# Kernel optimization log

Measured on AMD Instinct MI355X. Metric: run time of the kernel, lower is better.

The kernel has to match this reference:

```python
import jax, jax.numpy as jnp
import numpy as np

NUM_HEADS = 8

def setup_inputs() -> dict:
    key = jax.random.key(0)
    ks = jax.random.split(key, 6)
    B, nW, F_W, ED = 8, 64, 128, 512
    x = jax.random.normal(ks[0], (B * nW, F_W, ED), dtype=jnp.float32)
    adj_mask = jax.random.normal(ks[1], (B, NUM_HEADS, F_W, F_W), dtype=jnp.float32)
    qkv_w = jax.random.normal(ks[2], (ED, 3 * ED), dtype=jnp.float32) * (ED ** -0.5)
    qkv_b = jax.random.normal(ks[3], (3 * ED,), dtype=jnp.float32) * 0.02
    proj_w = jax.random.normal(ks[4], (ED, ED), dtype=jnp.float32) * (ED ** -0.5)
    proj_b = jax.random.normal(ks[5], (ED,), dtype=jnp.float32) * 0.02
    return {"x": x, "adj_mask": adj_mask, "qkv_w": qkv_w, "qkv_b": qkv_b,
            "proj_w": proj_w, "proj_b": proj_b, "B": B, "nW": nW}

def reference(x, adj_mask, qkv_w, qkv_b, proj_w, proj_b, B, nW):
    B_nW, F_W, ED = x.shape
    H = NUM_HEADS
    hd = ED // H
    scale = hd ** -0.5
    # qkv projection: [B_nW, F_W, 3, H, hd]
    qkv = (x @ qkv_w + qkv_b).reshape(B_nW, F_W, 3, H, hd)
    qkv = jnp.transpose(qkv, (2, 0, 3, 1, 4))  # [3, B_nW, H, F_W, hd]
    q, k, v = qkv[0], qkv[1], qkv[2]
    attn = jnp.einsum('bhqd,bhkd->bhqk', q * scale, k)  # [B_nW, H, F_W, F_W]
    # additive adjacency mask, broadcast over windows
    attn = attn.reshape(B, nW, H, F_W, F_W) + adj_mask[:, None]
    attn = attn.reshape(B_nW, H, F_W, F_W)
    attn = jax.nn.softmax(attn, axis=-1)
    out = jnp.einsum('bhqk,bhkd->bhqd', attn, v)  # [B_nW, H, F_W, hd]
    out = jnp.transpose(out, (0, 2, 1, 3)).reshape(B_nW, F_W, ED)
    return out @ proj_w + proj_b
```

## Files before the change

### kernel.cpp

```cpp
#include <hip/hip_runtime.h>

typedef __bf16 bf16_t;
typedef __bf16 bf16x8 __attribute__((ext_vector_type(8)));
typedef float f32x4 __attribute__((ext_vector_type(4)));
typedef float f32x16 __attribute__((ext_vector_type(16)));

#define MFMA16(a, b, c) __builtin_amdgcn_mfma_f32_16x16x32_bf16(a, b, c, 0, 0, 0)
#define MFMA32(a, b, c) __builtin_amdgcn_mfma_f32_32x32x16_bf16(a, b, c, 0, 0, 0)

#define F_W 128
#define ED 512
#define NH 8
#define HD 64
#define B_NW 512
#define NTOK 65536

typedef const __attribute__((address_space(1))) void gvoid_t;
typedef __attribute__((address_space(3))) void lvoid_t;
__device__ __forceinline__ void gload16(const void* g, void* l) {
    __builtin_amdgcn_global_load_lds((gvoid_t*)g, (lvoid_t*)l, 16, 0, 0);
}

__global__ __launch_bounds__(256) void prep_kernel(
    const float* __restrict__ qkv_w,
    const float* __restrict__ proj_w,
    bf16_t* __restrict__ qkv_wt,
    bf16_t* __restrict__ proj_wt) {
    int idx = blockIdx.x * 256 + threadIdx.x;
    if (idx < 1536 * 512) {
        int n = idx >> 9, k = idx & 511;
        qkv_wt[idx] = (bf16_t)qkv_w[k * 1536 + n];
    }
    if (idx < 512 * 512) {
        int n = idx >> 9, k = idx & 511;
        proj_wt[idx] = (bf16_t)proj_w[k * 512 + n];
    }
}

__global__ __launch_bounds__(256) void prep_x_kernel(
    const float* __restrict__ x, bf16_t* __restrict__ xbf) {
    size_t i = ((size_t)blockIdx.x * 256 + threadIdx.x) * 8;
    float4 v0 = *(const float4*)(x + i);
    float4 v1 = *(const float4*)(x + i + 4);
    bf16x8 o = {(bf16_t)v0.x, (bf16_t)v0.y, (bf16_t)v0.z, (bf16_t)v0.w,
                (bf16_t)v1.x, (bf16_t)v1.y, (bf16_t)v1.z, (bf16_t)v1.w};
    *(bf16x8*)(xbf + i) = o;
}

__global__ __launch_bounds__(256, 4) void qkv_gemm_kernel(
    const bf16_t* __restrict__ xbf,
    const bf16_t* __restrict__ qkv_wt,
    const float* __restrict__ qkv_b,
    bf16_t* qk_ws,
    bf16_t* vt_ws) {
    __shared__ __align__(16) char sm[32768];
    bf16_t* x_s = (bf16_t*)sm;
    bf16_t* w_s = (bf16_t*)(sm + 16384);
    bf16_t* tb  = (bf16_t*)sm;

    const int tid = threadIdx.x;
    const int wave = tid >> 6, lane = tid & 63;
    const int l31 = lane & 31, lhi = lane >> 5;
    const int wm = wave >> 1, wn = wave & 1;
    const int bid = blockIdx.x;
    const int idx = bid >> 3;
    const int mt_l = idx / 12;
    const int nt = idx - mt_l * 12;
    const int mtile = (bid & 7) * 64 + mt_l;
    const size_t m0 = (size_t)mtile * 128;
    const int n0 = nt * 128;

    const int srow = lane >> 3;
    const int scol = ((lane & 7) * 8) ^ ((srow & 7) << 3);

    f32x16 acc[2][2];
#pragma unroll
    for (int mf = 0; mf < 2; ++mf)
#pragma unroll
        for (int nf = 0; nf < 2; ++nf) acc[mf][nf] = (f32x16)0.0f;

    for (int kc = 0; kc < 8; ++kc) {
        const int k0 = kc * 64;
        __syncthreads();
#pragma unroll
        for (int i = 0; i < 4; ++i) {
            int c = wave * 4 + i;
            gload16(xbf + (m0 + c * 8 + srow) * 512 + k0 + scol, x_s + c * 512);
        }
#pragma unroll
        for (int i = 0; i < 4; ++i) {
            int c = wave * 4 + i;
            gload16(qkv_wt + (size_t)(n0 + c * 8 + srow) * 512 + k0 + scol,
                    w_s + c * 512);
        }
        __syncthreads();

#pragma unroll
        for (int ks = 0; ks < 4; ++ks) {
            bf16x8 a[2], b[2];
#pragma unroll
            for (int mf = 0; mf < 2; ++mf) {
                int row = wm * 64 + mf * 32 + l31;
                a[mf] = *(const bf16x8*)(x_s + row * 64 +
                                         ((ks * 16 + lhi * 8) ^ ((row & 7) << 3)));
            }
#pragma unroll
            for (int nf = 0; nf < 2; ++nf) {
                int rw = wn * 64 + nf * 32 + l31;
                b[nf] = *(const bf16x8*)(w_s + rw * 64 +
                                         ((ks * 16 + lhi * 8) ^ ((rw & 7) << 3)));
            }
#pragma unroll
            for (int mf = 0; mf < 2; ++mf)
#pragma unroll
                for (int nf = 0; nf < 2; ++nf)
                    acc[mf][nf] = MFMA32(a[mf], b[nf], acc[mf][nf]);
        }
    }

    if (nt < 8) {
        const float scale = (nt < 4) ? 0.125f : 1.0f;
#pragma unroll
        for (int nf = 0; nf < 2; ++nf) {
            int col = n0 + wn * 64 + nf * 32 + l31;
            float bv = qkv_b[col];
#pragma unroll
            for (int mf = 0; mf < 2; ++mf)
#pragma unroll
                for (int j = 0; j < 16; ++j) {
                    int r = wm * 64 + mf * 32 + (j & 3) + 8 * (j >> 2) + 4 * lhi;
                    qk_ws[(m0 + r) * 1024 + col] =
                        (bf16_t)((acc[mf][nf][j] + bv) * scale);
                }
        }
    } else {
#pragma unroll
        for (int hh = 0; hh < 2; ++hh) {
            int h = (nt - 8) * 2 + hh;
            __syncthreads();
            if (wn == hh) {
#pragma unroll
                for (int nf = 0; nf < 2; ++nf) {
                    int d = nf * 32 + l31;
                    float bv = qkv_b[n0 + hh * 64 + d];
#pragma unroll
                    for (int mf = 0; mf < 2; ++mf)
#pragma unroll
                        for (int j = 0; j < 16; ++j) {
                            int r = wm * 64 + mf * 32 + (j & 3) + 8 * (j >> 2) + 4 * lhi;
                            tb[r * 72 + d] = (bf16_t)(acc[mf][nf][j] + bv);
                        }
                }
            }
            __syncthreads();
            {
                int d = tid & 63;
                int kh = tid >> 6;
                bf16_t* outp = vt_ws + ((size_t)(mtile * 8 + h) * 64 + d) * 128 + kh * 32;
#pragma unroll
                for (int o = 0; o < 4; ++o) {
                    bf16x8 v;
#pragma unroll
                    for (int e = 0; e < 8; ++e)
                        v[e] = tb[(kh * 32 + o * 8 + e) * 72 + d];
                    *(bf16x8*)(outp + o * 8) = v;
                }
            }
        }
    }
}

__global__ __launch_bounds__(512, 4) void attn_kernel(
    bf16_t* qk_ws,
    const bf16_t* __restrict__ vt_ws,
    const float* __restrict__ adj) {
    __shared__ __align__(16) char sm[32768];
    bf16_t* k_lds  = (bf16_t*)sm;
    bf16_t* vt_lds = (bf16_t*)(sm + 16384);
    bf16_t* pbuf   = (bf16_t*)sm;

    const int tid = threadIdx.x;
    const int wave = tid >> 6, lane = tid & 63;
    const int lrow = lane & 15, lgrp = lane >> 4;
    const int bid = blockIdx.x;
    const int w = (bid & 7) * 64 + (bid >> 6);
    const int h = (bid >> 3) & 7;
    const int bidx = bid & 7;

    bf16_t* qrow = qk_ws + (size_t)w * 128 * 1024;

    {
        const int krow_l = lane >> 3;
        const int kcol_l = ((lane & 7) * 8) ^ ((krow_l & 7) << 3);
#pragma unroll
        for (int i = 0; i < 2; ++i) {
            int c = wave * 2 + i;
            gload16(qrow + (size_t)(c * 8 + krow_l) * 1024 + 512 + h * 64 + kcol_l,
                    k_lds + c * 512);
        }
    }
    {
        const bf16_t* vtb = vt_ws + (size_t)(w * 8 + h) * 64 * 128;
        const int vrow_l = lane >> 4;
#pragma unroll
        for (int i = 0; i < 2; ++i) {
            int c = wave * 2 + i;
            int d = c * 4 + vrow_l;
            int vcol = ((lane & 15) * 8) ^ ((d & 7) << 3);
            gload16(vtb + (size_t)d * 128 + vcol, vt_lds + c * 512);
        }
    }
    bf16x8 aq[2];
    {
        int row = wave * 16 + lrow;
#pragma unroll
        for (int kb = 0; kb < 2; ++kb)
            aq[kb] = *(const bf16x8*)(qrow + (size_t)row * 1024 + h * 64 + kb * 32 + lgrp * 8);
    }
    __syncthreads();

    f32x4 sacc[8];
#pragma unroll
    for (int nf = 0; nf < 8; ++nf) sacc[nf] = (f32x4)0.0f;
#pragma unroll
    for (int kb = 0; kb < 2; ++kb) {
        bf16x8 b[8];
#pragma unroll
        for (int nf = 0; nf < 8; ++nf) {
            int row = nf * 16 + lrow;
            b[nf] = *(const bf16x8*)(k_lds + row * 64 + ((kb * 32 + lgrp * 8) ^ ((row & 7) << 3)));
        }
#pragma unroll
        for (int nf = 0; nf < 8; ++nf)
            sacc[nf] = MFMA16(aq[kb], b[nf], sacc[nf]);
    }

    const float* mbase = adj + ((size_t)(bidx * NH + h)) * F_W * F_W;
#pragma unroll
    for (int j = 0; j < 4; ++j) {
        int row = wave * 16 + lgrp * 4 + j;
        const float* mrow = mbase + (size_t)row * F_W;
        float mx = -1e30f;
#pragma unroll
        for (int nf = 0; nf < 8; ++nf) {
            sacc[nf][j] += mrow[nf * 16 + lrow];
            mx = fmaxf(mx, sacc[nf][j]);
        }
#pragma unroll
        for (int d = 1; d < 16; d <<= 1) mx = fmaxf(mx, __shfl_xor(mx, d));
        float sum = 0.f;
#pragma unroll
        for (int nf = 0; nf < 8; ++nf) {
            float p = exp2f((sacc[nf][j] - mx) * 1.44269504f);
            sacc[nf][j] = p;
            sum += p;
        }
#pragma unroll
        for (int d = 1; d < 16; d <<= 1) sum += __shfl_xor(sum, d);
        float r = 1.0f / sum;
#pragma unroll
        for (int nf = 0; nf < 8; ++nf) sacc[nf][j] *= r;
    }
    __syncthreads();

    f32x4 oacc[4];
#pragma unroll
    for (int nf = 0; nf < 4; ++nf) oacc[nf] = (f32x4)0.0f;

#pragma unroll
    for (int kb = 0; kb < 4; ++kb) {
#pragma unroll
        for (int nn = 0; nn < 2; ++nn) {
            int nf = kb * 2 + nn;
            int kk = nn * 16 + lrow;
#pragma unroll
            for (int j = 0; j < 4; ++j) {
                int r = wave * 16 + lgrp * 4 + j;
                pbuf[r * 40 + kk] = (bf16_t)(sacc[nf][j]);
            }
        }
        __syncthreads();
        bf16x8 a = *(const bf16x8*)(pbuf + (wave * 16 + lrow) * 40 + lgrp * 8);
        bf16x8 b[4];
#pragma unroll
        for (int nf = 0; nf < 4; ++nf) {
            int d = nf * 16 + lrow;
            b[nf] = *(const bf16x8*)(vt_lds + d * 128 + ((kb * 32 + lgrp * 8) ^ ((d & 7) << 3)));
        }
#pragma unroll
        for (int nf = 0; nf < 4; ++nf)
            oacc[nf] = MFMA16(a, b[nf], oacc[nf]);
        __syncthreads();
    }

#pragma unroll
    for (int nf = 0; nf < 4; ++nf) {
        int ocol = h * 64 + nf * 16 + lrow;
#pragma unroll
        for (int j = 0; j < 4; ++j) {
            int r = wave * 16 + lgrp * 4 + j;
            qrow[(size_t)r * 1024 + ocol] = (bf16_t)oacc[nf][j];
        }
    }
}

__global__ __launch_bounds__(256, 4) void proj_kernel(
    const bf16_t* __restrict__ a_g,
    const bf16_t* __restrict__ bt_g,
    const float* __restrict__ bias,
    float* __restrict__ out) {
    __shared__ __align__(16) char sm_[32768];
    bf16_t* a_s = (bf16_t*)sm_;
    bf16_t* b_s = (bf16_t*)(sm_ + 16384);
    const int tid = threadIdx.x;
    const int wave = tid >> 6, lane = tid & 63;
    const int l31 = lane & 31, lhi = lane >> 5;
    const int wm = wave >> 1, wn = wave & 1;
    const int bid = blockIdx.x;
    const int mtile = (bid & 7) * 64 + (bid >> 5);
    const int ntile = (bid >> 3) & 3;
    const size_t m0 = (size_t)mtile * 128;
    const int n0 = ntile * 128;
    const int srow = lane >> 3;
    const int scol = ((lane & 7) * 8) ^ ((srow & 7) << 3);

    f32x16 acc[2][2];
#pragma unroll
    for (int mf = 0; mf < 2; ++mf)
#pragma unroll
        for (int nf = 0; nf < 2; ++nf) acc[mf][nf] = (f32x16)0.0f;

    for (int kc = 0; kc < 8; ++kc) {
        const int k0 = kc * 64;
        __syncthreads();
#pragma unroll
        for (int i = 0; i < 4; ++i) {
            int c = wave * 4 + i;
            gload16(a_g + (m0 + c * 8 + srow) * 1024 + k0 + scol, a_s + c * 512);
            gload16(bt_g + (size_t)(n0 + c * 8 + srow) * 512 + k0 + scol, b_s + c * 512);
        }
        __syncthreads();

#pragma unroll
        for (int ks = 0; ks < 4; ++ks) {
            bf16x8 a[2], b[2];
#pragma unroll
            for (int mf = 0; mf < 2; ++mf) {
                int row = wm * 64 + mf * 32 + l31;
                a[mf] = *(const bf16x8*)(a_s + row * 64 +
                                         ((ks * 16 + lhi * 8) ^ ((row & 7) << 3)));
            }
#pragma unroll
            for (int nf = 0; nf < 2; ++nf) {
                int rw = wn * 64 + nf * 32 + l31;
                b[nf] = *(const bf16x8*)(b_s + rw * 64 +
                                         ((ks * 16 + lhi * 8) ^ ((rw & 7) << 3)));
            }
#pragma unroll
            for (int mf = 0; mf < 2; ++mf)
#pragma unroll
                for (int nf = 0; nf < 2; ++nf)
                    acc[mf][nf] = MFMA32(a[mf], b[nf], acc[mf][nf]);
        }
    }

#pragma unroll
    for (int nf = 0; nf < 2; ++nf) {
        int col = n0 + wn * 64 + nf * 32 + l31;
        float bv = bias[col];
#pragma unroll
        for (int mf = 0; mf < 2; ++mf)
#pragma unroll
            for (int j = 0; j < 16; ++j) {
                size_t row = m0 + wm * 64 + mf * 32 + (j & 3) + 8 * (j >> 2) + 4 * lhi;
                out[row * 512 + col] = acc[mf][nf][j] + bv;
            }
    }
}

extern "C" void kernel_launch(void* const* d_in, const int* in_sizes, int n_in,
                              void* d_out, int out_size, void* d_ws, size_t ws_size,
                              hipStream_t stream) {
    const float* x      = (const float*)d_in[0];
    const float* adj    = (const float*)d_in[1];
    const float* qkv_w  = (const float*)d_in[2];
    const float* qkv_b  = (const float*)d_in[3];
    const float* proj_w = (const float*)d_in[4];
    const float* proj_b = (const float*)d_in[5];
    float* out = (float*)d_out;

    bf16_t* qk_ws   = (bf16_t*)d_ws;
    bf16_t* vt_ws   = qk_ws + (size_t)NTOK * 1024;
    bf16_t* qkv_wt  = vt_ws + (size_t)4096 * 64 * 128;
    bf16_t* proj_wt = qkv_wt + 1536 * 512;
    bf16_t* xbf = (bf16_t*)d_out;

    prep_kernel<<<3072, 256, 0, stream>>>(qkv_w, proj_w, qkv_wt, proj_wt);
    prep_x_kernel<<<NTOK * ED / 8 / 256, 256, 0, stream>>>(x, xbf);
    qkv_gemm_kernel<<<6144, 256, 0, stream>>>(xbf, qkv_wt, qkv_b, qk_ws, vt_ws);
    attn_kernel<<<4096, 512, 0, stream>>>(qk_ws, vt_ws, adj);
    proj_kernel<<<2048, 256, 0, stream>>>(qk_ws, proj_wt, proj_b, out);
}
```

Measured before the change: 294.7 us.

## Enlarge QKV and projection GEMM tiles to 256x256 with double-buffered LDS

Both GEMM kernels move from 128x128 tiles with 4 waves to 256x256 tiles with 8 waves, each wave computing a 128x64 sub-tile. K-chunks are double-buffered in 128KB of LDS, so the global-to-LDS load of the next chunk overlaps the MFMA work on the current one, and only one barrier is needed per iteration. The LDS layout is split into 32-column halves with a new swizzle. The larger tiles cut redundant global traffic, but they raise register and LDS pressure and lower occupancy. The V-transpose epilogue now spans two windows per tile.

```diff
diff --git a/kernel.cpp b/kernel.cpp
--- a/kernel.cpp
+++ b/kernel.cpp
@@ -12,13 +12,17 @@
 #define ED 512
 #define NH 8
 #define HD 64
-#define B_NW 512
 #define NTOK 65536
 
 typedef const __attribute__((address_space(1))) void gvoid_t;
 typedef __attribute__((address_space(3))) void lvoid_t;
 __device__ __forceinline__ void gload16(const void* g, void* l) {
     __builtin_amdgcn_global_load_lds((gvoid_t*)g, (lvoid_t*)l, 16, 0, 0);
+}
+
+__device__ __forceinline__ int swz32(int row) { return ((row >> 1) & 3) << 3; }
+__device__ __forceinline__ int drow(int j, int lhi) {
+    return (j & 3) + 8 * (j >> 2) + 4 * lhi;
 }
 
 __global__ __launch_bounds__(256) void prep_kernel(
@@ -47,107 +51,117 @@
     *(bf16x8*)(xbf + i) = o;
 }
 
-__global__ __launch_bounds__(256, 4) void qkv_gemm_kernel(
+__global__ __launch_bounds__(512, 2) void qkv_gemm_kernel(
     const bf16_t* __restrict__ xbf,
     const bf16_t* __restrict__ qkv_wt,
     const float* __restrict__ qkv_b,
     bf16_t* qk_ws,
     bf16_t* vt_ws) {
-    __shared__ __align__(16) char sm[32768];
-    bf16_t* x_s = (bf16_t*)sm;
-    bf16_t* w_s = (bf16_t*)(sm + 16384);
-    bf16_t* tb  = (bf16_t*)sm;
+    __shared__ __align__(16) char smem[131072];
+    bf16_t* tb = (bf16_t*)smem;
 
     const int tid = threadIdx.x;
     const int wave = tid >> 6, lane = tid & 63;
     const int l31 = lane & 31, lhi = lane >> 5;
-    const int wm = wave >> 1, wn = wave & 1;
+    const int wm = wave >> 2;
+    const int wn = wave & 3;
     const int bid = blockIdx.x;
     const int idx = bid >> 3;
-    const int mt_l = idx / 12;
-    const int nt = idx - mt_l * 12;
-    const int mtile = (bid & 7) * 64 + mt_l;
-    const size_t m0 = (size_t)mtile * 128;
-    const int n0 = nt * 128;
-
-    const int srow = lane >> 3;
-    const int scol = ((lane & 7) * 8) ^ ((srow & 7) << 3);
-
-    f32x16 acc[2][2];
-#pragma unroll
-    for (int mf = 0; mf < 2; ++mf)
+    const int mt_l = idx / 6;
+    const int nt = idx - mt_l * 6;
+    const int mtile = (bid & 7) * 32 + mt_l;
+    const size_t m0 = (size_t)mtile * 256;
+    const int n0 = nt * 256;
+
+    const int row16 = lane >> 2;
+    const int scol = ((lane & 3) * 8) ^ swz32(row16);
+
+    f32x16 acc[4][2];
+#pragma unroll
+    for (int mf = 0; mf < 4; ++mf)
 #pragma unroll
         for (int nf = 0; nf < 2; ++nf) acc[mf][nf] = (f32x16)0.0f;
 
+#define STAGE_QKV(buf, k0)                                                     \
+    {                                                                          \
+        char* _b = (buf);                                                      \
+        int c = wave * 2;                                                      \
+        _Pragma("unroll") for (int s = 0; s < 2; ++s) {                        \
+            _Pragma("unroll") for (int i = 0; i < 2; ++i) {                    \
+                gload16(xbf + (m0 + (c + i) * 16 + row16) * 512 + (k0) + s * 32 + scol, \
+                        (bf16_t*)(_b + s * 16384) + (c + i) * 512);            \
+                gload16(qkv_wt + (size_t)(n0 + (c + i) * 16 + row16) * 512 + (k0) + s * 32 + scol, \
+                        (bf16_t*)(_b + 32768 + s * 16384) + (c + i) * 512);    \
+            }                                                                  \
+        }                                                                      \
+    }
+
+    STAGE_QKV(smem, 0);
+    __syncthreads();
+
+#pragma unroll 2
     for (int kc = 0; kc < 8; ++kc) {
-        const int k0 = kc * 64;
-        __syncthreads();
-#pragma unroll
-        for (int i = 0; i < 4; ++i) {
-            int c = wave * 4 + i;
-            gload16(xbf + (m0 + c * 8 + srow) * 512 + k0 + scol, x_s + c * 512);
-        }
-#pragma unroll
-        for (int i = 0; i < 4; ++i) {
-            int c = wave * 4 + i;
-            gload16(qkv_wt + (size_t)(n0 + c * 8 + srow) * 512 + k0 + scol,
-                    w_s + c * 512);
-        }
-        __syncthreads();
-
+        char* cur = smem + (kc & 1) * 65536;
+        char* nxt = smem + ((kc & 1) ^ 1) * 65536;
+        if (kc < 7) STAGE_QKV(nxt, (kc + 1) * 64);
 #pragma unroll
         for (int ks = 0; ks < 4; ++ks) {
-            bf16x8 a[2], b[2];
-#pragma unroll
-            for (int mf = 0; mf < 2; ++mf) {
-                int row = wm * 64 + mf * 32 + l31;
-                a[mf] = *(const bf16x8*)(x_s + row * 64 +
-                                         ((ks * 16 + lhi * 8) ^ ((row & 7) << 3)));
+            const int kk = ks >> 1, kslot = ks & 1;
+            bf16_t* as = (bf16_t*)(cur + kk * 16384);
+            bf16_t* bs = (bf16_t*)(cur + 32768 + kk * 16384);
+            bf16x8 a[4], b[2];
+#pragma unroll
+            for (int mf = 0; mf < 4; ++mf) {
+                int row = wm * 128 + mf * 32 + l31;
+                a[mf] = *(const bf16x8*)(as + row * 32 +
+                                         ((kslot * 16 + lhi * 8) ^ swz32(row)));
             }
 #pragma unroll
             for (int nf = 0; nf < 2; ++nf) {
                 int rw = wn * 64 + nf * 32 + l31;
-                b[nf] = *(const bf16x8*)(w_s + rw * 64 +
-                                         ((ks * 16 + lhi * 8) ^ ((rw & 7) << 3)));
-            }
-#pragma unroll
-            for (int mf = 0; mf < 2; ++mf)
+                b[nf] = *(const bf16x8*)(bs + rw * 32 +
+                                         ((kslot * 16 + lhi * 8) ^ swz32(rw)));
+            }
+#pragma unroll
+            for (int mf = 0; mf < 4; ++mf)
 #pragma unroll
                 for (int nf = 0; nf < 2; ++nf)
                     acc[mf][nf] = MFMA32(a[mf], b[nf], acc[mf][nf]);
         }
-    }
-
-    if (nt < 8) {
-        const float scale = (nt < 4) ? 0.125f : 1.0f;
+        __syncthreads();
+    }
+#undef STAGE_QKV
+
+    if (nt < 4) {
+        const float scale = (nt < 2) ? 0.125f : 1.0f;
 #pragma unroll
         for (int nf = 0; nf < 2; ++nf) {
             int col = n0 + wn * 64 + nf * 32 + l31;
             float bv = qkv_b[col];
 #pragma unroll
-            for (int mf = 0; mf < 2; ++mf)
+            for (int mf = 0; mf < 4; ++mf)
 #pragma unroll
                 for (int j = 0; j < 16; ++j) {
-                    int r = wm * 64 + mf * 32 + (j & 3) + 8 * (j >> 2) + 4 * lhi;
+                    int r = wm * 128 + mf * 32 + drow(j, lhi);
                     qk_ws[(m0 + r) * 1024 + col] =
                         (bf16_t)((acc[mf][nf][j] + bv) * scale);
                 }
         }
     } else {
 #pragma unroll
-        for (int hh = 0; hh < 2; ++hh) {
-            int h = (nt - 8) * 2 + hh;
+        for (int hh = 0; hh < 4; ++hh) {
+            int h = (nt - 4) * 4 + hh;
             __syncthreads();
             if (wn == hh) {
 #pragma unroll
                 for (int nf = 0; nf < 2; ++nf) {
                     int d = nf * 32 + l31;
-                    float bv = qkv_b[n0 + hh * 64 + d];
-#pragma unroll
-                    for (int mf = 0; mf < 2; ++mf)
+                    float bv = qkv_b[1024 + (nt - 4) * 256 + hh * 64 + d];
+#pragma unroll
+                    for (int mf = 0; mf < 4; ++mf)
 #pragma unroll
                         for (int j = 0; j < 16; ++j) {
-                            int r = wm * 64 + mf * 32 + (j & 3) + 8 * (j >> 2) + 4 * lhi;
+                            int r = wm * 128 + mf * 32 + drow(j, lhi);
                             tb[r * 72 + d] = (bf16_t)(acc[mf][nf][j] + bv);
                         }
                 }
@@ -156,14 +170,16 @@
             {
                 int d = tid & 63;
                 int kh = tid >> 6;
-                bf16_t* outp = vt_ws + ((size_t)(mtile * 8 + h) * 64 + d) * 128 + kh * 32;
 #pragma unroll
                 for (int o = 0; o < 4; ++o) {
+                    int k = kh * 32 + o * 8;
+                    int win = mtile * 2 + (k >> 7);
                     bf16x8 v;
 #pragma unroll
                     for (int e = 0; e < 8; ++e)
-                        v[e] = tb[(kh * 32 + o * 8 + e) * 72 + d];
-                    *(bf16x8*)(outp + o * 8) = v;
+                        v[e] = tb[(k + e) * 72 + d];
+                    *(bf16x8*)(vt_ws + ((size_t)(win * 8 + h) * 64 + d) * 128 +
+                               (k & 127)) = v;
                 }
             }
         }
@@ -304,75 +320,90 @@
     }
 }
 
-__global__ __launch_bounds__(256, 4) void proj_kernel(
+__global__ __launch_bounds__(512, 2) void proj_kernel(
     const bf16_t* __restrict__ a_g,
     const bf16_t* __restrict__ bt_g,
     const float* __restrict__ bias,
     float* __restrict__ out) {
-    __shared__ __align__(16) char sm_[32768];
-    bf16_t* a_s = (bf16_t*)sm_;
-    bf16_t* b_s = (bf16_t*)(sm_ + 16384);
+    __shared__ __align__(16) char smem[131072];
     const int tid = threadIdx.x;
     const int wave = tid >> 6, lane = tid & 63;
     const int l31 = lane & 31, lhi = lane >> 5;
-    const int wm = wave >> 1, wn = wave & 1;
+    const int wm = wave >> 2, wn = wave & 3;
     const int bid = blockIdx.x;
-    const int mtile = (bid & 7) * 64 + (bid >> 5);
-    const int ntile = (bid >> 3) & 3;
-    const size_t m0 = (size_t)mtile * 128;
-    const int n0 = ntile * 128;
-    const int srow = lane >> 3;
-    const int scol = ((lane & 7) * 8) ^ ((srow & 7) << 3);
-
-    f32x16 acc[2][2];
-#pragma unroll
-    for (int mf = 0; mf < 2; ++mf)
+    const int idx = bid >> 3;
+    const int mtile = (bid & 7) * 32 + (idx >> 1);
+    const int ntile = idx & 1;
+    const size_t m0 = (size_t)mtile * 256;
+    const int n0 = ntile * 256;
+    const int row16 = lane >> 2;
+    const int scol = ((lane & 3) * 8) ^ swz32(row16);
+
+    f32x16 acc[4][2];
+#pragma unroll
+    for (int mf = 0; mf < 4; ++mf)
 #pragma unroll
         for (int nf = 0; nf < 2; ++nf) acc[mf][nf] = (f32x16)0.0f;
 
+#define STAGE_PROJ(buf, k0)                                                    \
+    {                                                                          \
+        char* _b = (buf);                                                      \
+        int c = wave * 2;                                                      \
+        _Pragma("unroll") for (int s = 0; s < 2; ++s) {                        \
+            _Pragma("unroll") for (int i = 0; i < 2; ++i) {                    \
+                gload16(a_g + (m0 + (c + i) * 16 + row16) * 1024 + (k0) + s * 32 + scol, \
+                        (bf16_t*)(_b + s * 16384) + (c + i) * 512);            \
+                gload16(bt_g + (size_t)(n0 + (c + i) * 16 + row16) * 512 + (k0) + s * 32 + scol, \
+                        (bf16_t*)(_b + 32768 + s * 16384) + (c + i) * 512);    \
+            }                                                                  \
+        }                                                                      \
+    }
+
+    STAGE_PROJ(smem, 0);
+    __syncthreads();
+
+#pragma unroll 2
     for (int kc = 0; kc < 8; ++kc) {
-        const int k0 = kc * 64;
-        __syncthreads();
-#pragma unroll
-        for (int i = 0; i < 4; ++i) {
-            int c = wave * 4 + i;
-            gload16(a_g + (m0 + c * 8 + srow) * 1024 + k0 + scol, a_s + c * 512);
-            gload16(bt_g + (size_t)(n0 + c * 8 + srow) * 512 + k0 + scol, b_s + c * 512);
-        }
-        __syncthreads();
-
+        char* cur = smem + (kc & 1) * 65536;
+        char* nxt = smem + ((kc & 1) ^ 1) * 65536;
+        if (kc < 7) STAGE_PROJ(nxt, (kc + 1) * 64);
 #pragma unroll
         for (int ks = 0; ks < 4; ++ks) {
-            bf16x8 a[2], b[2];
-#pragma unroll
-            for (int mf = 0; mf < 2; ++mf) {
-                int row = wm * 64 + mf * 32 + l31;
-                a[mf] = *(const bf16x8*)(a_s + row * 64 +
-                                         ((ks * 16 + lhi * 8) ^ ((row & 7) << 3)));
+            const int kk = ks >> 1, kslot = ks & 1;
+            bf16_t* as = (bf16_t*)(cur + kk * 16384);
+            bf16_t* bs = (bf16_t*)(cur + 32768 + kk * 16384);
+            bf16x8 a[4], b[2];
+#pragma unroll
+            for (int mf = 0; mf < 4; ++mf) {
+                int row = wm * 128 + mf * 32 + l31;
+                a[mf] = *(const bf16x8*)(as + row * 32 +
+                                         ((kslot * 16 + lhi * 8) ^ swz32(row)));
             }
 #pragma unroll
             for (int nf = 0; nf < 2; ++nf) {
                 int rw = wn * 64 + nf * 32 + l31;
-                b[nf] = *(const bf16x8*)(b_s + rw * 64 +
-                                         ((ks * 16 + lhi * 8) ^ ((rw & 7) << 3)));
-            }
-#pragma unroll
-            for (int mf = 0; mf < 2; ++mf)
+                b[nf] = *(const bf16x8*)(bs + rw * 32 +
+                                         ((kslot * 16 + lhi * 8) ^ swz32(rw)));
+            }
+#pragma unroll
+            for (int mf = 0; mf < 4; ++mf)
 #pragma unroll
                 for (int nf = 0; nf < 2; ++nf)
                     acc[mf][nf] = MFMA32(a[mf], b[nf], acc[mf][nf]);
         }
-    }
+        __syncthreads();
+    }
+#undef STAGE_PROJ
 
 #pragma unroll
     for (int nf = 0; nf < 2; ++nf) {
         int col = n0 + wn * 64 + nf * 32 + l31;
         float bv = bias[col];
 #pragma unroll
-        for (int mf = 0; mf < 2; ++mf)
+        for (int mf = 0; mf < 4; ++mf)
 #pragma unroll
             for (int j = 0; j < 16; ++j) {
-                size_t row = m0 + wm * 64 + mf * 32 + (j & 3) + 8 * (j >> 2) + 4 * lhi;
+                size_t row = m0 + wm * 128 + mf * 32 + drow(j, lhi);
                 out[row * 512 + col] = acc[mf][nf][j] + bv;
             }
     }
@@ -397,7 +428,7 @@
 
     prep_kernel<<<3072, 256, 0, stream>>>(qkv_w, proj_w, qkv_wt, proj_wt);
     prep_x_kernel<<<NTOK * ED / 8 / 256, 256, 0, stream>>>(x, xbf);
-    qkv_gemm_kernel<<<6144, 256, 0, stream>>>(xbf, qkv_wt, qkv_b, qk_ws, vt_ws);
+    qkv_gemm_kernel<<<1536, 512, 0, stream>>>(xbf, qkv_wt, qkv_b, qk_ws, vt_ws);
     attn_kernel<<<4096, 512, 0, stream>>>(qk_ws, vt_ws, adj);
-    proj_kernel<<<2048, 256, 0, stream>>>(qk_ws, proj_wt, proj_b, out);
-}
+    proj_kernel<<<512, 512, 0, stream>>>(qk_ws, proj_wt, proj_b, out);
+}
```

Result: slower. 319.5 us (+8.4%).
